# Kernel tuning notes

Hardware: AMD Instinct MI355X
Metric: run time of the kernel (lower is better)

Reference implementation:

```python
import jax, jax.numpy as jnp
import numpy as np

E = 384      # hidden_dim
H = 8        # num_attention_heads
D = E // H   # head_dim = 48


def setup_inputs() -> dict:
    key = jax.random.key(0)
    ks = jax.random.split(key, 11)
    B, S = 4, 2048
    patch_embeds = jax.random.normal(ks[0], (B, S, E), dtype=jnp.float32)
    attention_mask = jax.random.randint(ks[1], (B, S), 0, 2).astype(bool)
    s = 1.0 / np.sqrt(E)
    Wq = jax.random.normal(ks[2], (E, E), dtype=jnp.float32) * s
    bq = jnp.zeros((E,), dtype=jnp.float32)
    Wk = jax.random.normal(ks[3], (E, E), dtype=jnp.float32) * s
    bk = jnp.zeros((E,), dtype=jnp.float32)
    Wv = jax.random.normal(ks[4], (E, E), dtype=jnp.float32) * s
    bv = jnp.zeros((E,), dtype=jnp.float32)
    Wo = jax.random.normal(ks[5], (E, E), dtype=jnp.float32) * s
    bo = jnp.zeros((E,), dtype=jnp.float32)
    return {"patch_embeds": patch_embeds, "attention_mask": attention_mask,
            "Wq": Wq, "bq": bq, "Wk": Wk, "bk": bk,
            "Wv": Wv, "bv": bv, "Wo": Wo, "bo": bo}


def reference(patch_embeds, attention_mask, Wq, bq, Wk, bk, Wv, bv, Wo, bo):
    B, S, _ = patch_embeds.shape
    scale = D ** (-0.5)
    # QKV projections (nn.Linear: x @ W.T + b); W stored as [out,in]
    q = patch_embeds @ Wq.T + bq
    k = patch_embeds @ Wk.T + bk
    v = patch_embeds @ Wv.T + bv
    # [B,S,E] -> [B,H,S,D]
    q = q.reshape(B, S, H, D).transpose(0, 2, 1, 3)
    k = k.reshape(B, S, H, D).transpose(0, 2, 1, 3)
    v = v.reshape(B, S, H, D).transpose(0, 2, 1, 3)
    # scaled dot-product attention with key mask (True = masked)
    scores = jnp.einsum('bhqd,bhkd->bhqk', q, k) * scale
    mask = attention_mask[:, None, None, :]  # [B,1,1,S]
    scores = jnp.where(mask, -jnp.inf, scores)
    weights = jax.nn.softmax(scores, axis=-1)
    out = jnp.einsum('bhqk,bhkd->bhqd', weights, v)
    out = out.transpose(0, 2, 1, 3).reshape(B, S, E)
    return out @ Wo.T + bo
```

## Files before the change

kernel.cpp:

```cpp
#include <hip/hip_runtime.h>
#include <math.h>

#define B_ 4
#define S_ 2048
#define E_ 384
#define H_ 8
#define D_ 48
#define M_ (B_*S_)
#define DP_ 64
constexpr float QK_SCALE = 0.14433756729740643f * 1.4426950408889634f;

typedef __attribute__((ext_vector_type(8))) short short8;
typedef __attribute__((ext_vector_type(4))) float f32x4;
typedef unsigned short u16;

__device__ inline u16 f2bf(float f) {
    unsigned u = __float_as_uint(f);
    return (u16)((u + 0x7FFFu + ((u >> 16) & 1u)) >> 16);
}
__device__ inline float bf2f(u16 h) { return __uint_as_float(((unsigned)h) << 16); }
__device__ inline unsigned pk2(float a, float b) {
    return (unsigned)f2bf(a) | ((unsigned)f2bf(b) << 16);
}
__device__ inline unsigned pk2_fast(float a, float b) {
#if __has_builtin(__builtin_amdgcn_perm)
    unsigned ua = __float_as_uint(a) + 0x8000u;
    unsigned ub = __float_as_uint(b) + 0x8000u;
    return __builtin_amdgcn_perm(ub, ua, 0x07060302u);
#else
    return pk2(a, b);
#endif
}
__device__ inline float fexp2(float x) {
#if __has_builtin(__builtin_amdgcn_exp2f)
    return __builtin_amdgcn_exp2f(x);
#else
    return exp2f(x);
#endif
}
__device__ inline void glld16(const void* g, void* l) {
    __builtin_amdgcn_global_load_lds((const __attribute__((address_space(1))) unsigned int*)g,
                                     (__attribute__((address_space(3))) unsigned int*)l, 16, 0, 0);
}

__global__ __launch_bounds__(256) void prep(const float4* __restrict__ x,
                                            const int* __restrict__ mask,
                                            const float4* __restrict__ wq,
                                            const float4* __restrict__ wk,
                                            const float4* __restrict__ wv,
                                            const float4* __restrict__ wo,
                                            uint2* __restrict__ xb,
                                            uint2* __restrict__ wb,
                                            u16* __restrict__ Qp, u16* __restrict__ Kp) {
    const int bx = blockIdx.x, t = threadIdx.x;
    if (bx < 3072) {
        int i = bx * 256 + t;
        float4 v = x[i];
        uint2 H;
        H.x = pk2(v.x, v.y);
        H.y = pk2(v.z, v.w);
        xb[i] = H;
    } else if (bx < 3072 + 144) {
        int i = (bx - 3072) * 256 + t;
        const int n4 = 36864;
        const float4* srcs[4] = {wq, wk, wv, wo};
        #pragma unroll
        for (int j = 0; j < 4; ++j) {
            float4 v = srcs[j][i];
            uint2 H;
            H.x = pk2(v.x, v.y);
            H.y = pk2(v.z, v.w);
            wb[(size_t)j * n4 + i] = H;
        }
    } else {
        int i = (bx - 3216) * 256 + t;
        int bh = i >> 11, s = i & 2047, b = bh >> 3;
        size_t off = ((size_t)bh * S_ + s) * DP_ + 48;
        uint4 qz = {0x00004300u, 0, 0, 0};
        uint4 kz = {mask[b * S_ + s] ? 0x0000BF80u : 0u, 0, 0, 0};
        uint4 z  = {0, 0, 0, 0};
        *reinterpret_cast<uint4*>(Qp + off)     = qz;
        *reinterpret_cast<uint4*>(Qp + off + 8) = z;
        *reinterpret_cast<uint4*>(Kp + off)     = kz;
        *reinterpret_cast<uint4*>(Kp + off + 8) = z;
    }
}

__global__ __launch_bounds__(256) void gemm_qkv3(const u16* __restrict__ xb,
                                                 const u16* __restrict__ wb,
                                                 const float* __restrict__ bq,
                                                 const float* __restrict__ bk,
                                                 const float* __restrict__ bv,
                                                 u16* __restrict__ Qp, u16* __restrict__ Kp,
                                                 u16* __restrict__ Vtp) {
    __shared__ u16 smem[4 * 4096];
    u16* As = smem;

    const int t = threadIdx.x, w = t >> 6, lane = t & 63;
    const int ln = lane & 15, quad = lane >> 4;
    const int gr = lane >> 3;
    const int gc = (lane & 7) ^ gr;
    const int m0 = blockIdx.x * 64;
    const int n0 = blockIdx.y * 64;
    const int b  = m0 >> 11;

    f32x4 acc[3][4];
    #pragma unroll
    for (int j = 0; j < 3; ++j)
        #pragma unroll
        for (int nt = 0; nt < 4; ++nt)
            acc[j][nt] = (f32x4){0.f, 0.f, 0.f, 0.f};

    for (int kk = 0; kk < 384; kk += 64) {
        __syncthreads();
        #pragma unroll
        for (int i = 0; i < 2; ++i) {
            int r0 = w * 16 + i * 8;
            glld16(xb + (size_t)(m0 + r0 + gr) * E_ + kk + gc * 8, As + r0 * 64);
        }
        #pragma unroll
        for (int j = 0; j < 3; ++j)
            #pragma unroll
            for (int i = 0; i < 2; ++i) {
                int r0 = w * 16 + i * 8;
                glld16(wb + (size_t)j * 147456 + (size_t)(n0 + r0 + gr) * E_ + kk + gc * 8,
                       smem + (1 + j) * 4096 + r0 * 64);
            }
        __syncthreads();

        #pragma unroll
        for (int ks = 0; ks < 2; ++ks) {
            const int slot = (ks * 4 + quad) ^ (ln & 7);
            short8 ah = *reinterpret_cast<const short8*>(&As[(w * 16 + ln) * 64 + slot * 8]);
            #pragma unroll
            for (int j = 0; j < 3; ++j) {
                const u16* Wsj = smem + (1 + j) * 4096;
                #pragma unroll
                for (int nt = 0; nt < 4; ++nt) {
                    short8 wf = *reinterpret_cast<const short8*>(&Wsj[(nt * 16 + ln) * 64 + slot * 8]);
                    acc[j][nt] = __builtin_amdgcn_mfma_f32_16x16x32_bf16(ah, wf, acc[j][nt], 0, 0, 0);
                }
            }
        }
    }

    {
        const int s_base = (m0 & 2047) + w * 16 + quad * 4;
        #pragma unroll
        for (int nt = 0; nt < 4; ++nt) {
            const int col = n0 + nt * 16 + ln;
            const int h   = (col * 683) >> 15;
            const int d   = col - h * 48;
            const float bc = bv[col];
            u16* dst = Vtp + ((size_t)(b * 8 + h) * 48 + d) * 2048;
            uint2 pk;
            pk.x = pk2(acc[2][nt][0] + bc, acc[2][nt][1] + bc);
            pk.y = pk2(acc[2][nt][2] + bc, acc[2][nt][3] + bc);
            *reinterpret_cast<uint2*>(dst + s_base) = pk;
        }
    }

    u16* TrQ = smem;
    u16* TrK = smem + 64 * 76;
    __syncthreads();
    #pragma unroll
    for (int nt = 0; nt < 4; ++nt) {
        const int col = n0 + nt * 16 + ln;
        const float bcq = bq[col], bck = bk[col];
        #pragma unroll
        for (int r = 0; r < 4; ++r) {
            int row = w * 16 + quad * 4 + r;
            TrQ[row * 76 + nt * 16 + ln] = f2bf((acc[0][nt][r] + bcq) * QK_SCALE);
            TrK[row * 76 + nt * 16 + ln] = f2bf(acc[1][nt][r] + bck);
        }
    }
    __syncthreads();
    {
        const int row = t >> 2, quarter = t & 3;
        const int s   = (m0 & 2047) + row;
        #pragma unroll
        for (int c = 0; c < 2; ++c) {
            int gcol = n0 + quarter * 16 + c * 8;
            int h = (gcol * 683) >> 15;
            int d = gcol - h * 48;
            size_t off = ((size_t)(b * 8 + h) * 2048 + s) * DP_ + d;
            *reinterpret_cast<uint4*>(Qp + off) =
                *reinterpret_cast<const uint4*>(&TrQ[row * 76 + quarter * 16 + c * 8]);
            *reinterpret_cast<uint4*>(Kp + off) =
                *reinterpret_cast<const uint4*>(&TrK[row * 76 + quarter * 16 + c * 8]);
        }
    }
}

__global__ __launch_bounds__(256) void gemm_out(const u16* __restrict__ ab,
                                                const u16* __restrict__ wb,
                                                const float* __restrict__ bo, float* __restrict__ out) {
    __shared__ u16 smem[2 * 4096 + 2 * 4096];
    u16* As = smem;
    u16* Ws = smem + 2 * 4096;
    const int t = threadIdx.x, w = t >> 6, lane = t & 63;
    const int ln = lane & 15, quad = lane >> 4;
    const int gr = lane >> 3;
    const int gc = (lane & 7) ^ gr;
    const int m0 = blockIdx.x * 64, n0 = blockIdx.y * 64;
    const u16* wh = wb + (size_t)3 * 147456;

    f32x4 acc[4];
    #pragma unroll
    for (int nt = 0; nt < 4; ++nt) acc[nt] = (f32x4){0.f, 0.f, 0.f, 0.f};

    auto stage = [&](int bf, int kk) {
        #pragma unroll
        for (int i = 0; i < 2; ++i) {
            int r0 = w * 16 + i * 8;
            glld16(ab + (size_t)(m0 + r0 + gr) * E_ + kk + gc * 8, As + bf * 4096 + r0 * 64);
            glld16(wh + (size_t)(n0 + r0 + gr) * E_ + kk + gc * 8, Ws + bf * 4096 + r0 * 64);
        }
    };

    stage(0, 0);
    __syncthreads();
    #pragma unroll
    for (int it = 0; it < 6; ++it) {
        const int cur = it & 1;
        if (it < 5) stage(cur ^ 1, (it + 1) * 64);
        const u16* Ab = As + cur * 4096;
        const u16* Wb = Ws + cur * 4096;
        #pragma unroll
        for (int ks = 0; ks < 2; ++ks) {
            const int slot = (ks * 4 + quad) ^ (ln & 7);
            short8 ah = *reinterpret_cast<const short8*>(&Ab[(w * 16 + ln) * 64 + slot * 8]);
            #pragma unroll
            for (int nt = 0; nt < 4; ++nt) {
                short8 wf = *reinterpret_cast<const short8*>(&Wb[(nt * 16 + ln) * 64 + slot * 8]);
                acc[nt] = __builtin_amdgcn_mfma_f32_16x16x32_bf16(ah, wf, acc[nt], 0, 0, 0);
            }
        }
        __syncthreads();
    }

    #pragma unroll
    for (int nt = 0; nt < 4; ++nt) {
        const int col = n0 + nt * 16 + ln;
        const float bc = bo[col];
        #pragma unroll
        for (int r = 0; r < 4; ++r) {
            size_t row = (size_t)(m0 + w * 16 + quad * 4 + r);
            out[row * E_ + col] = acc[nt][r] + bc;
        }
    }
}

__global__ __launch_bounds__(256, 2) void attn_mfma(const u16* __restrict__ Qp,
                                                    const u16* __restrict__ Kp,
                                                    const u16* __restrict__ Vtp,
                                                    u16* __restrict__ AO) {
    __shared__ __align__(16) u16 QPs[128 * 64];
    __shared__ __align__(16) u16 Ksh[2][64 * 64];
    __shared__ __align__(16) u16 Vt[2][48 * 64];
    __shared__ float linv[4][32];

    const int t    = threadIdx.x;
    const int w    = t >> 6;
    const int lane = t & 63;
    const int ln   = lane & 15;
    const int quad = lane >> 4;
    const int gr   = lane >> 3;
    const int gc   = (lane & 7) ^ gr;
    const int bh   = blockIdx.x;
    const int q0   = blockIdx.y * 128;
    const int b    = bh >> 3, h = bh & 7;
    const int cb   = h * 48;
    const size_t rb = (size_t)b * S_;

    const u16* Qsrc = Qp  + ((size_t)bh * S_ + q0) * DP_;
    const u16* Ksrc = Kp  + (size_t)bh * S_ * DP_;
    const u16* Vsrc = Vtp + (size_t)bh * 48 * 2048;

    const int swz0 = ((quad    ) ^ (ln & 7)) << 3;
    const int swz1 = ((4 + quad) ^ (ln & 7)) << 3;
    const u16* kA[2][2], *vA[2][2];
    #pragma unroll
    for (int bf = 0; bf < 2; ++bf) {
        kA[bf][0] = &Ksh[bf][ln * 64 + swz0];
        kA[bf][1] = &Ksh[bf][ln * 64 + swz1];
        vA[bf][0] = &Vt[bf][ln * 64 + swz0];
        vA[bf][1] = &Vt[bf][ln * 64 + swz1];
    }
    int qrow[2];
    const u16 *pR[2][2];
    u16* pW[2][4];
    #pragma unroll
    for (int qt = 0; qt < 2; ++qt) {
        qrow[qt] = (w * 32 + qt * 16 + ln) * 64;
        pR[qt][0] = &QPs[qrow[qt] + swz0];
        pR[qt][1] = &QPs[qrow[qt] + swz1];
        #pragma unroll
        for (int Mt = 0; Mt < 4; ++Mt)
            pW[qt][Mt] = &QPs[qrow[qt] +
                ((((Mt * 2 + (quad >> 1)) ^ (ln & 7)) << 3) | ((quad & 1) << 2))];
    }

    auto stage = [&](int bf, int kt) {
        const int k0 = kt * 64;
        glld16(Ksrc + (size_t)(k0 + w * 16 + gr) * DP_ + gc * 8,     &Ksh[bf][(w * 16) * 64]);
        glld16(Ksrc + (size_t)(k0 + w * 16 + 8 + gr) * DP_ + gc * 8, &Ksh[bf][(w * 16 + 8) * 64]);
        if (w < 3) {
            glld16(Vsrc + (size_t)(w * 16 + gr) * 2048 + k0 + gc * 8,     &Vt[bf][(w * 16) * 64]);
            glld16(Vsrc + (size_t)(w * 16 + 8 + gr) * 2048 + k0 + gc * 8, &Vt[bf][(w * 16 + 8) * 64]);
        }
    };

    #pragma unroll
    for (int i = 0; i < 4; ++i) {
        int r0 = w * 32 + i * 8;
        glld16(Qsrc + (size_t)(r0 + gr) * DP_ + gc * 8, &QPs[r0 * 64]);
    }
    stage(0, 0);
    __syncthreads();

    short8 qf[2][2];
    #pragma unroll
    for (int qt = 0; qt < 2; ++qt) {
        qf[qt][0] = *reinterpret_cast<const short8*>(pR[qt][0]);
        qf[qt][1] = *reinterpret_cast<const short8*>(pR[qt][1]);
    }

    f32x4 o[2][3];
    #pragma unroll
    for (int qt = 0; qt < 2; ++qt)
        #pragma unroll
        for (int nt = 0; nt < 3; ++nt) o[qt][nt] = (f32x4){0.f, 0.f, 0.f, 0.f};
    float lq[2] = {0.f, 0.f};

    auto body = [&](int cur, int nxt, int ktn) {
        if (ktn < 32) stage(nxt, ktn);

        f32x4 sc[4][2];
        #pragma unroll
        for (int Mt = 0; Mt < 4; ++Mt) {
            short8 kf0 = *reinterpret_cast<const short8*>(kA[cur][0] + Mt * 1024);
            short8 kf1 = *reinterpret_cast<const short8*>(kA[cur][1] + Mt * 1024);
            #pragma unroll
            for (int qt = 0; qt < 2; ++qt) {
                f32x4 a0 = __builtin_amdgcn_mfma_f32_16x16x32_bf16(kf0, qf[qt][0], (f32x4){0.f,0.f,0.f,0.f}, 0, 0, 0);
                sc[Mt][qt] = __builtin_amdgcn_mfma_f32_16x16x32_bf16(kf1, qf[qt][1], a0, 0, 0, 0);
            }
        }

        #pragma unroll
        for (int qt = 0; qt < 2; ++qt)
            #pragma unroll
            for (int Mt = 0; Mt < 4; ++Mt) {
                float p0 = fexp2(sc[Mt][qt][0]);
                float p1 = fexp2(sc[Mt][qt][1]);
                float p2 = fexp2(sc[Mt][qt][2]);
                float p3 = fexp2(sc[Mt][qt][3]);
                lq[qt] += (p0 + p1) + (p2 + p3);
                uint2 pk;
                pk.x = pk2_fast(p0, p1);
                pk.y = pk2_fast(p2, p3);
                *reinterpret_cast<uint2*>(pW[qt][Mt]) = pk;
            }

        short8 pa[2][2];
        #pragma unroll
        for (int qt = 0; qt < 2; ++qt) {
            pa[qt][0] = *reinterpret_cast<const short8*>(pR[qt][0]);
            pa[qt][1] = *reinterpret_cast<const short8*>(pR[qt][1]);
        }
        #pragma unroll
        for (int nt = 0; nt < 3; ++nt) {
            short8 vb0 = *reinterpret_cast<const short8*>(vA[cur][0] + nt * 1024);
            short8 vb1 = *reinterpret_cast<const short8*>(vA[cur][1] + nt * 1024);
            #pragma unroll
            for (int qt = 0; qt < 2; ++qt) {
                o[qt][nt] = __builtin_amdgcn_mfma_f32_16x16x32_bf16(pa[qt][0], vb0, o[qt][nt], 0, 0, 0);
                o[qt][nt] = __builtin_amdgcn_mfma_f32_16x16x32_bf16(pa[qt][1], vb1, o[qt][nt], 0, 0, 0);
            }
        }
        __syncthreads();
    };

    for (int kt = 0; kt < 32; kt += 2) {
        body(0, 1, kt + 1);
        body(1, 0, kt + 2);
    }

    #pragma unroll
    for (int qt = 0; qt < 2; ++qt) {
        float l = lq[qt];
        l += __shfl_xor(l, 16);
        l += __shfl_xor(l, 32);
        if (quad == 0) linv[w][qt * 16 + ln] = 1.0f / l;
    }
    __syncthreads();
    #pragma unroll
    for (int qt = 0; qt < 2; ++qt) {
        f32x4 il = *reinterpret_cast<const f32x4*>(&linv[w][qt * 16 + quad * 4]);
        #pragma unroll
        for (int nt = 0; nt < 3; ++nt)
            #pragma unroll
            for (int r = 0; r < 4; ++r) {
                size_t row = rb + q0 + w * 32 + qt * 16 + quad * 4 + r;
                size_t idx = row * E_ + cb + nt * 16 + ln;
                AO[idx] = f2bf(o[qt][nt][r] * il[r]);
            }
    }
}

extern "C" void kernel_launch(void* const* d_in, const int* in_sizes, int n_in,
                              void* d_out, int out_size, void* d_ws, size_t ws_size,
                              hipStream_t stream) {
    (void)in_sizes; (void)n_in; (void)out_size; (void)ws_size;
    const float* x    = (const float*)d_in[0];
    const int*   mask = (const int*)  d_in[1];
    const float* Wq   = (const float*)d_in[2];
    const float* bq   = (const float*)d_in[3];
    const float* Wk   = (const float*)d_in[4];
    const float* bk   = (const float*)d_in[5];
    const float* Wv   = (const float*)d_in[6];
    const float* bv   = (const float*)d_in[7];
    const float* Wo   = (const float*)d_in[8];
    const float* bo   = (const float*)d_in[9];

    const size_t NELEM = (size_t)M_ * E_;
    const size_t WELEM = (size_t)E_ * E_;
    const size_t PEL   = (size_t)B_ * H_ * S_ * DP_;
    u16* ws = (u16*)d_ws;
    u16* xb  = ws;
    u16* wb  = xb + NELEM;
    u16* Qp  = wb + 4 * WELEM;
    u16* Kp  = Qp + PEL;
    u16* Vtp = Kp + PEL;
    u16* AO  = xb;

    dim3 blk(256);
    prep<<<dim3(3472), blk, 0, stream>>>(
        (const float4*)x, mask,
        (const float4*)Wq, (const float4*)Wk, (const float4*)Wv, (const float4*)Wo,
        (uint2*)xb, (uint2*)wb, Qp, Kp);

    gemm_qkv3<<<dim3(M_ / 64, 6), blk, 0, stream>>>(xb, wb, bq, bk, bv, Qp, Kp, Vtp);

    attn_mfma<<<dim3(B_ * H_, S_ / 128), blk, 0, stream>>>(Qp, Kp, Vtp, AO);

    gemm_out<<<dim3(M_ / 64, 6), blk, 0, stream>>>(AO, wb, bo, (float*)d_out);
}
```

Measured before the change: 147.5 us.

## Load K/V fragments directly from global into registers, dropping LDS staging

The attention kernel no longer stages K and V tiles through double-buffered shared memory with async global-to-LDS loads and block barriers. Each wave now reads its own Q, K and V MFMA fragments straight from global memory (relying on L1/L2 for reuse across the four waves), and only P goes through LDS. This removes the __syncthreads per tile and frees LDS, which may allow more occupancy. In exchange every wave issues redundant global loads of K/V, there is no explicit prefetch, and it drops barriers around P writes/reads in shared memory (each wave touches only its own rows, so this is likely safe).

```diff
diff --git a/kernel.cpp b/kernel.cpp
--- a/kernel.cpp
+++ b/kernel.cpp
@@ -255,9 +255,7 @@
                                                     const u16* __restrict__ Kp,
                                                     const u16* __restrict__ Vtp,
                                                     u16* __restrict__ AO) {
-    __shared__ __align__(16) u16 QPs[128 * 64];
-    __shared__ __align__(16) u16 Ksh[2][64 * 64];
-    __shared__ __align__(16) u16 Vt[2][48 * 64];
+    __shared__ __align__(16) u16 Ps[128 * 64];
     __shared__ float linv[4][32];
 
     const int t    = threadIdx.x;
@@ -265,66 +263,38 @@
     const int lane = t & 63;
     const int ln   = lane & 15;
     const int quad = lane >> 4;
-    const int gr   = lane >> 3;
-    const int gc   = (lane & 7) ^ gr;
     const int bh   = blockIdx.x;
     const int q0   = blockIdx.y * 128;
     const int b    = bh >> 3, h = bh & 7;
     const int cb   = h * 48;
     const size_t rb = (size_t)b * S_;
 
-    const u16* Qsrc = Qp  + ((size_t)bh * S_ + q0) * DP_;
+    const u16* Qsrc = Qp  + ((size_t)bh * S_ + q0 + w * 32) * DP_;
     const u16* Ksrc = Kp  + (size_t)bh * S_ * DP_;
     const u16* Vsrc = Vtp + (size_t)bh * 48 * 2048;
 
     const int swz0 = ((quad    ) ^ (ln & 7)) << 3;
     const int swz1 = ((4 + quad) ^ (ln & 7)) << 3;
-    const u16* kA[2][2], *vA[2][2];
-    #pragma unroll
-    for (int bf = 0; bf < 2; ++bf) {
-        kA[bf][0] = &Ksh[bf][ln * 64 + swz0];
-        kA[bf][1] = &Ksh[bf][ln * 64 + swz1];
-        vA[bf][0] = &Vt[bf][ln * 64 + swz0];
-        vA[bf][1] = &Vt[bf][ln * 64 + swz1];
-    }
-    int qrow[2];
     const u16 *pR[2][2];
     u16* pW[2][4];
     #pragma unroll
     for (int qt = 0; qt < 2; ++qt) {
-        qrow[qt] = (w * 32 + qt * 16 + ln) * 64;
-        pR[qt][0] = &QPs[qrow[qt] + swz0];
-        pR[qt][1] = &QPs[qrow[qt] + swz1];
+        const int qrow = (w * 32 + qt * 16 + ln) * 64;
+        pR[qt][0] = &Ps[qrow + swz0];
+        pR[qt][1] = &Ps[qrow + swz1];
         #pragma unroll
         for (int Mt = 0; Mt < 4; ++Mt)
-            pW[qt][Mt] = &QPs[qrow[qt] +
+            pW[qt][Mt] = &Ps[qrow +
                 ((((Mt * 2 + (quad >> 1)) ^ (ln & 7)) << 3) | ((quad & 1) << 2))];
     }
 
-    auto stage = [&](int bf, int kt) {
-        const int k0 = kt * 64;
-        glld16(Ksrc + (size_t)(k0 + w * 16 + gr) * DP_ + gc * 8,     &Ksh[bf][(w * 16) * 64]);
-        glld16(Ksrc + (size_t)(k0 + w * 16 + 8 + gr) * DP_ + gc * 8, &Ksh[bf][(w * 16 + 8) * 64]);
-        if (w < 3) {
-            glld16(Vsrc + (size_t)(w * 16 + gr) * 2048 + k0 + gc * 8,     &Vt[bf][(w * 16) * 64]);
-            glld16(Vsrc + (size_t)(w * 16 + 8 + gr) * 2048 + k0 + gc * 8, &Vt[bf][(w * 16 + 8) * 64]);
-        }
-    };
-
-    #pragma unroll
-    for (int i = 0; i < 4; ++i) {
-        int r0 = w * 32 + i * 8;
-        glld16(Qsrc + (size_t)(r0 + gr) * DP_ + gc * 8, &QPs[r0 * 64]);
-    }
-    stage(0, 0);
-    __syncthreads();
-
     short8 qf[2][2];
     #pragma unroll
-    for (int qt = 0; qt < 2; ++qt) {
-        qf[qt][0] = *reinterpret_cast<const short8*>(pR[qt][0]);
-        qf[qt][1] = *reinterpret_cast<const short8*>(pR[qt][1]);
-    }
+    for (int qt = 0; qt < 2; ++qt)
+        #pragma unroll
+        for (int ks = 0; ks < 2; ++ks)
+            qf[qt][ks] = *reinterpret_cast<const short8*>(
+                Qsrc + (size_t)(qt * 16 + ln) * DP_ + ks * 32 + quad * 8);
 
     f32x4 o[2][3];
     #pragma unroll
@@ -333,20 +303,32 @@
         for (int nt = 0; nt < 3; ++nt) o[qt][nt] = (f32x4){0.f, 0.f, 0.f, 0.f};
     float lq[2] = {0.f, 0.f};
 
-    auto body = [&](int cur, int nxt, int ktn) {
-        if (ktn < 32) stage(nxt, ktn);
+    for (int kt = 0; kt < 32; ++kt) {
+        const int k0 = kt * 64;
+
+        short8 kf[4][2];
+        #pragma unroll
+        for (int Mt = 0; Mt < 4; ++Mt)
+            #pragma unroll
+            for (int ks = 0; ks < 2; ++ks)
+                kf[Mt][ks] = *reinterpret_cast<const short8*>(
+                    Ksrc + (size_t)(k0 + Mt * 16 + ln) * DP_ + ks * 32 + quad * 8);
+        short8 vb[3][2];
+        #pragma unroll
+        for (int nt = 0; nt < 3; ++nt)
+            #pragma unroll
+            for (int ks = 0; ks < 2; ++ks)
+                vb[nt][ks] = *reinterpret_cast<const short8*>(
+                    Vsrc + (size_t)(nt * 16 + ln) * 2048 + k0 + ks * 32 + quad * 8);
 
         f32x4 sc[4][2];
         #pragma unroll
-        for (int Mt = 0; Mt < 4; ++Mt) {
-            short8 kf0 = *reinterpret_cast<const short8*>(kA[cur][0] + Mt * 1024);
-            short8 kf1 = *reinterpret_cast<const short8*>(kA[cur][1] + Mt * 1024);
+        for (int Mt = 0; Mt < 4; ++Mt)
             #pragma unroll
             for (int qt = 0; qt < 2; ++qt) {
-                f32x4 a0 = __builtin_amdgcn_mfma_f32_16x16x32_bf16(kf0, qf[qt][0], (f32x4){0.f,0.f,0.f,0.f}, 0, 0, 0);
-                sc[Mt][qt] = __builtin_amdgcn_mfma_f32_16x16x32_bf16(kf1, qf[qt][1], a0, 0, 0, 0);
-            }
-        }
+                f32x4 a0 = __builtin_amdgcn_mfma_f32_16x16x32_bf16(kf[Mt][0], qf[qt][0], (f32x4){0.f,0.f,0.f,0.f}, 0, 0, 0);
+                sc[Mt][qt] = __builtin_amdgcn_mfma_f32_16x16x32_bf16(kf[Mt][1], qf[qt][1], a0, 0, 0, 0);
+            }
 
         #pragma unroll
         for (int qt = 0; qt < 2; ++qt)
@@ -370,21 +352,12 @@
             pa[qt][1] = *reinterpret_cast<const short8*>(pR[qt][1]);
         }
         #pragma unroll
-        for (int nt = 0; nt < 3; ++nt) {
-            short8 vb0 = *reinterpret_cast<const short8*>(vA[cur][0] + nt * 1024);
-            short8 vb1 = *reinterpret_cast<const short8*>(vA[cur][1] + nt * 1024);
+        for (int nt = 0; nt < 3; ++nt)
             #pragma unroll
             for (int qt = 0; qt < 2; ++qt) {
-                o[qt][nt] = __builtin_amdgcn_mfma_f32_16x16x32_bf16(pa[qt][0], vb0, o[qt][nt], 0, 0, 0);
-                o[qt][nt] = __builtin_amdgcn_mfma_f32_16x16x32_bf16(pa[qt][1], vb1, o[qt][nt], 0, 0, 0);
-            }
-        }
-        __syncthreads();
-    };
-
-    for (int kt = 0; kt < 32; kt += 2) {
-        body(0, 1, kt + 1);
-        body(1, 0, kt + 2);
+                o[qt][nt] = __builtin_amdgcn_mfma_f32_16x16x32_bf16(pa[qt][0], vb[nt][0], o[qt][nt], 0, 0, 0);
+                o[qt][nt] = __builtin_amdgcn_mfma_f32_16x16x32_bf16(pa[qt][1], vb[nt][1], o[qt][nt], 0, 0, 0);
+            }
     }
 
     #pragma unroll
```

Result: slower. 207.0 us (+40.3%).
